# Kernel tuning notes

Measured on AMD Instinct MI355X. Metric: run time of the kernel, lower is better.

## Reference

```python
import jax, jax.numpy as jnp
import numpy as np

N_NODES = 10000
N_EDGES = 640000
NF = 64    # node_feature_size
EF = 64    # edge_feature_size
NH = 128   # node_hidden_size
EH = 128   # edge_hidden_size
CS = 128   # context_size


def _linear_init(key, fan_in, shape):
    bound = 1.0 / np.sqrt(fan_in)
    return jax.random.uniform(key, shape, jnp.float32, -bound, bound)


def setup_inputs() -> dict:
    key = jax.random.key(0)
    ks = jax.random.split(key, 20)
    node_feats = jax.random.normal(ks[0], (N_NODES, NF), jnp.float32)
    edge_feats = jax.random.normal(ks[1], (N_EDGES, EF), jnp.float32)
    src = jax.random.randint(ks[2], (N_EDGES,), 0, N_NODES, jnp.int32)
    dst = jax.random.randint(ks[3], (N_EDGES,), 0, N_NODES, jnp.int32)
    return {
        "node_feats": node_feats,
        "edge_feats": edge_feats,
        "W_node": _linear_init(ks[4], NF, (NF, NH)),
        "b_node": _linear_init(ks[5], NF, (NH,)),
        "W_edge": _linear_init(ks[6], NF + EF, (NF + EF, EH)),
        "b_edge": _linear_init(ks[7], NF + EF, (EH,)),
        "W_logit": _linear_init(ks[8], NH + EH, (NH + EH, 1)),
        "b_logit": _linear_init(ks[9], NH + EH, (1,)),
        "W_msg": _linear_init(ks[10], EH, (EH, CS)),
        "b_msg": _linear_init(ks[11], EH, (CS,)),
        "W_ih": _linear_init(ks[12], NH, (3 * NH, CS)),   # torch GRUCell weight_ih layout
        "W_hh": _linear_init(ks[13], NH, (3 * NH, NH)),
        "b_ih": _linear_init(ks[14], NH, (3 * NH,)),
        "b_hh": _linear_init(ks[15], NH, (3 * NH,)),
        "src": src,
        "dst": dst,
    }


def reference(node_feats, edge_feats, W_node, b_node, W_edge, b_edge,
              W_logit, b_logit, W_msg, b_msg, W_ih, W_hh, b_ih, b_hh,
              src, dst):
    n_nodes = node_feats.shape[0]
    # (1) embed nodes: h_v = LeakyReLU(Linear(f_v))
    h_v = jax.nn.leaky_relu(node_feats @ W_node + b_node)          # [N, NH]
    # (2) embed edges from [src node feats, edge feats]
    e_in = jnp.concatenate([node_feats[src], edge_feats], axis=1)  # [M, NF+EF]
    h_e = jax.nn.leaky_relu(e_in @ W_edge + b_edge)                # [M, EH]
    # raw messages T(h_w->v)
    m = h_e @ W_msg + b_msg                                        # [M, CS]
    # (3) attention logits from [src node hidden, edge hidden]
    l_in = jnp.concatenate([h_v[src], h_e], axis=1)                # [M, NH+EH]
    logit = jax.nn.leaky_relu(l_in @ W_logit + b_logit)            # [M, 1]
    # (4) edge softmax grouped by destination node
    lmax = jax.ops.segment_max(logit, dst, num_segments=n_nodes)   # [N, 1]
    ex = jnp.exp(logit - lmax[dst])
    den = jax.ops.segment_sum(ex, dst, num_segments=n_nodes)       # [N, 1]
    alpha = ex / den[dst]                                          # [M, 1]
    # (5) weighted segment-sum context, then elu
    C_v = jax.ops.segment_sum(alpha * m, dst, num_segments=n_nodes)  # [N, CS]
    C_v = jax.nn.elu(C_v)
    # (6) GRUCell(input=C_v, hidden=h_v), torch semantics, then ReLU
    gi = C_v @ W_ih.T + b_ih                                       # [N, 3*NH]
    gh = h_v @ W_hh.T + b_hh
    i_r, i_z, i_n = jnp.split(gi, 3, axis=1)
    h_r, h_z, h_n = jnp.split(gh, 3, axis=1)
    r = jax.nn.sigmoid(i_r + h_r)
    z = jax.nn.sigmoid(i_z + h_z)
    n = jnp.tanh(i_n + r * h_n)
    h_new = jax.nn.relu((1.0 - z) * n + z * h_v)                   # [N, NH]
    # update_edges=False -> return original edge feats alongside new node states
    return h_new, edge_feats
```

## Files before the change

kernel.cpp:

```cpp
#include <hip/hip_runtime.h>
#include <hip/hip_bf16.h>

typedef unsigned short u16;
typedef unsigned int u32;

typedef __attribute__((ext_vector_type(8))) short bf16x8;
typedef __attribute__((ext_vector_type(4))) float f32x4;

__device__ __forceinline__ u16 f2bf(float f) {
    u32 u = __float_as_uint(f);
    u32 r = ((u >> 16) & 1u) + 0x7fffu;
    return (u16)((u + r) >> 16);
}
__device__ __forceinline__ float bf2f(u16 u) {
    return __uint_as_float(((u32)u) << 16);
}
__device__ __forceinline__ float leaky(float x) { return x >= 0.f ? x : 0.01f * x; }

__global__ __launch_bounds__(256) void k_prep_transpose(
    const float* __restrict__ We, u16* __restrict__ WeT)
{
    int idx = blockIdx.x * 256 + threadIdx.x;
    int r = (idx >> 7) & 127;
    int c = idx & 127;
    WeT[c * 128 + r] = f2bf(We[r * 128 + c]);
}

__global__ __launch_bounds__(256) void k_csr_count(
    const int* __restrict__ dst, u32* __restrict__ deg, int nE)
{
    long e = (long)blockIdx.x * 256 + threadIdx.x;
    if (e >= nE) return;
    atomicAdd(&deg[dst[e]], 1u);
}

__global__ __launch_bounds__(256) void k_csr_scan(
    const u32* __restrict__ deg, u32* __restrict__ start,
    u32* __restrict__ cur, int nN)
{
    __shared__ u32 s[256];
    int t = threadIdx.x;
    int chunk = (nN + 255) / 256;
    int a = t * chunk;
    int b = a + chunk; if (b > nN) b = nN; if (a > nN) a = nN;
    u32 sum = 0;
    for (int i = a; i < b; i++) sum += deg[i];
    s[t] = sum;
    __syncthreads();
    for (int d = 1; d < 256; d <<= 1) {
        u32 v = (t >= d) ? s[t - d] : 0u;
        __syncthreads();
        s[t] += v;
        __syncthreads();
    }
    u32 base = (t == 0) ? 0u : s[t - 1];
    for (int i = a; i < b; i++) { start[i] = base; cur[i] = base; base += deg[i]; }
}

__global__ __launch_bounds__(256) void k_csr_scatter(
    const int* __restrict__ src, const int* __restrict__ dst,
    u32* __restrict__ cur, int* __restrict__ sEidG,
    int* __restrict__ sSrcG, int* __restrict__ sDstG, int nE)
{
    long e = (long)blockIdx.x * 256 + threadIdx.x;
    if (e >= nE) return;
    int d = dst[e];
    u32 p = atomicAdd(&cur[d], 1u);
    sEidG[p] = (int)e;
    sSrcG[p] = src[e];
    sDstG[p] = d;
}

__global__ __launch_bounds__(128) void k_node_embed(
    const float* __restrict__ nf, const float* __restrict__ Wn,
    const float* __restrict__ bn, const float* __restrict__ WL,
    float* __restrict__ h_v, float* __restrict__ g, int nN)
{
    __shared__ float sW[64][128];
    __shared__ float sF[8][64];
    __shared__ float sRed[2][8];
    int j = threadIdx.x;
    int n0 = blockIdx.x * 8;
    for (int i = 0; i < 64; i++) sW[i][j] = Wn[i * 128 + j];
    for (int t = j; t < 8 * 64; t += 128) {
        int n = t >> 6, k = t & 63;
        int nn = n0 + n; if (nn >= nN) nn = nN - 1;
        sF[n][k] = nf[(long)nn * 64 + k];
    }
    __syncthreads();
    float bj = bn[j];
    float wl = WL[j];
    int wv = j >> 6, ln = j & 63;
    float hval[8];
    for (int n = 0; n < 8; n++) {
        float acc = bj;
        #pragma unroll 16
        for (int k = 0; k < 64; k++) acc += sF[n][k] * sW[k][j];
        float h = leaky(acc);
        hval[n] = h;
        if (n0 + n < nN) h_v[(long)(n0 + n) * 128 + j] = h;
    }
    #pragma unroll
    for (int n = 0; n < 8; n++) {
        float part = hval[n] * wl;
        #pragma unroll
        for (int o = 1; o < 64; o <<= 1) part += __shfl_xor(part, o);
        if (ln == 0) sRed[wv][n] = part;
    }
    __syncthreads();
    if (j < 8 && n0 + j < nN) g[n0 + j] = sRed[0][j] + sRed[1][j];
}

template<bool WRITE_HE>
__global__ __launch_bounds__(256, 4) void k_edge_logit(
    const float* __restrict__ nf, const float* __restrict__ ef,
    const int* __restrict__ sEidG, const int* __restrict__ sSrcG,
    const u16* __restrict__ WeT, const float* __restrict__ be,
    const float* __restrict__ WL, const float* __restrict__ bL,
    const float* __restrict__ g,
    float* __restrict__ logitS, u16* __restrict__ heG,
    float* __restrict__ efOut, int nE)
{
    __shared__ u16 sW[64][136];
    __shared__ u16 sIn[64][136];
    __shared__ float sWL2[128];
    __shared__ float sG[64];
    __shared__ int sSrc[64];
    __shared__ int sEid[64];
    int tid = threadIdx.x;
    long p0 = (long)blockIdx.x * 64;
    if (tid < 64) {
        long p = p0 + tid; if (p >= nE) p = nE - 1;
        int eid = sEidG[p];
        int s = sSrcG[p];
        sEid[tid] = eid;
        sSrc[tid] = s;
        sG[tid] = g[s];
    } else if (tid < 192) {
        sWL2[tid - 64] = WL[64 + tid];
    }
    __syncthreads();
    for (int c = tid; c < 1024; c += 256) {
        int r = c >> 4, p = c & 15;
        *((uint4*)&sW[r][p * 8]) = *((const uint4*)(WeT + r * 128 + p * 8));
    }
    for (int c = tid; c < 2048; c += 256) {
        int e = c >> 5, p = c & 31;
        float4 v;
        if (p < 16) {
            v = *((const float4*)(nf + (long)sSrc[e] * 64 + p * 4));
        } else {
            v = *((const float4*)(ef + (long)sEid[e] * 64 + (p - 16) * 4));
            if (p0 + e < nE)
                *((float4*)(efOut + (long)sEid[e] * 64 + (p - 16) * 4)) = v;
        }
        u32 lo = (u32)f2bf(v.x) | ((u32)f2bf(v.y) << 16);
        u32 hi = (u32)f2bf(v.z) | ((u32)f2bf(v.w) << 16);
        *((u32*)&sIn[e][p * 4])     = lo;
        *((u32*)&sIn[e][p * 4 + 2]) = hi;
    }
    __syncthreads();

    int lane = tid & 63, w = tid >> 6;
    int nl = lane & 15, q = lane >> 4;
    int eA = w * 16 + nl;
    bf16x8 afr[4];
    #pragma unroll
    for (int s = 0; s < 4; s++)
        afr[s] = *((const bf16x8*)&sIn[eA][s * 32 + q * 8]);
    f32x4 acc[8];
    #pragma unroll
    for (int t = 0; t < 8; t++) acc[t] = (f32x4){0.f, 0.f, 0.f, 0.f};
    #pragma unroll
    for (int s = 0; s < 4; s++) {
        int k0 = s * 32 + q * 8;
        #pragma unroll
        for (int t = 0; t < 4; t++) {
            bf16x8 b = *((const bf16x8*)&sW[t * 16 + nl][k0]);
            acc[t] = __builtin_amdgcn_mfma_f32_16x16x32_bf16(afr[s], b, acc[t], 0, 0, 0);
        }
    }
    __syncthreads();
    for (int c = tid; c < 1024; c += 256) {
        int r = c >> 4, p = c & 15;
        *((uint4*)&sW[r][p * 8]) = *((const uint4*)(WeT + (64 + r) * 128 + p * 8));
    }
    __syncthreads();
    #pragma unroll
    for (int s = 0; s < 4; s++) {
        int k0 = s * 32 + q * 8;
        #pragma unroll
        for (int t = 0; t < 4; t++) {
            bf16x8 b = *((const bf16x8*)&sW[t * 16 + nl][k0]);
            acc[4 + t] = __builtin_amdgcn_mfma_f32_16x16x32_bf16(afr[s], b, acc[4 + t], 0, 0, 0);
        }
    }
    #pragma unroll
    for (int t = 0; t < 8; t++) {
        int col = t * 16 + nl;
        float bias = be[col];
        #pragma unroll
        for (int r = 0; r < 4; r++) {
            int e = w * 16 + q * 4 + r;
            sIn[e][col] = f2bf(leaky(acc[t][r] + bias));
        }
    }
    if (WRITE_HE) {
        #pragma unroll
        for (int i = 0; i < 4; i++) {
            int row = w * 16 + i * 4 + (lane >> 4);
            int ch = lane & 15;
            long pg = p0 + row;
            uint4 v4 = *((const uint4*)&sIn[row][ch * 8]);
            if (pg < nE) *((uint4*)(heG + pg * 128 + ch * 8)) = v4;
        }
    }
    int ew = lane >> 2, sub = lane & 3;
    int e = w * 16 + ew;
    float sum = 0.f;
    #pragma unroll
    for (int i = 0; i < 4; i++) {
        bf16x8 hv = *((const bf16x8*)&sIn[e][sub * 32 + i * 8]);
        #pragma unroll
        for (int jj = 0; jj < 8; jj++)
            sum += bf2f((u16)hv[jj]) * sWL2[sub * 32 + i * 8 + jj];
    }
    sum += __shfl_xor(sum, 1);
    sum += __shfl_xor(sum, 2);
    if (sub == 0 && p0 + e < nE) {
        float l = leaky(sum + sG[e] + bL[0]);
        logitS[p0 + e] = l;
    }
}

__global__ __launch_bounds__(256) void k_softmax_msg(
    const u32* __restrict__ start, const u32* __restrict__ deg,
    const u16* __restrict__ heG, float* __restrict__ logitS,
    float* __restrict__ A, int nN)
{
    __shared__ float sAl[4][1024];
    int wv = threadIdx.x >> 6, lane = threadIdx.x & 63;
    int v = blockIdx.x * 4 + wv;
    if (v >= nN) return;
    long base = (long)v * 128;
    u32 d = deg[v];
    if (d == 0) {
        A[base + lane] = 0.f;
        A[base + lane + 64] = 0.f;
        return;
    }
    u32 s0 = start[v];
    float mx = -3.402823e38f;
    for (u32 i = lane; i < d; i += 64) mx = fmaxf(mx, logitS[s0 + i]);
    #pragma unroll
    for (int o = 1; o < 64; o <<= 1) mx = fmaxf(mx, __shfl_xor(mx, o));
    float sum = 0.f;
    for (u32 i = lane; i < d; i += 64) {
        float e_ = __expf(logitS[s0 + i] - mx);
        sum += e_;
        if (i < 1024) sAl[wv][i] = e_;
        else logitS[s0 + i] = e_;
    }
    #pragma unroll
    for (int o = 1; o < 64; o <<= 1) sum += __shfl_xor(sum, o);
    float inv = 1.f / sum;
    float ax = 0.f, ay = 0.f;
    #pragma unroll 4
    for (u32 i = 0; i < d; i++) {
        float al = (i < 1024) ? sAl[wv][i] : logitS[s0 + i];
        u32 rw = *((const u32*)(heG + ((long)(s0 + i)) * 128 + lane * 2));
        ax += al * bf2f((u16)(rw & 0xffffu));
        ay += al * bf2f((u16)(rw >> 16));
    }
    A[base + lane * 2]     = ax * inv;
    A[base + lane * 2 + 1] = ay * inv;
}

__global__ __launch_bounds__(256) void k_softmax_node(
    const u32* __restrict__ start, const u32* __restrict__ deg,
    float* __restrict__ logitS, int nN)
{
    int v = blockIdx.x * 4 + (threadIdx.x >> 6);
    int lane = threadIdx.x & 63;
    if (v >= nN) return;
    u32 d = deg[v];
    if (d == 0) return;
    u32 s0 = start[v];
    float mx = -3.402823e38f;
    for (u32 i = lane; i < d; i += 64) mx = fmaxf(mx, logitS[s0 + i]);
    #pragma unroll
    for (int o = 1; o < 64; o <<= 1) mx = fmaxf(mx, __shfl_xor(mx, o));
    float sum = 0.f;
    for (u32 i = lane; i < d; i += 64) {
        float e = __expf(logitS[s0 + i] - mx);
        logitS[s0 + i] = e;
        sum += e;
    }
    #pragma unroll
    for (int o = 1; o < 64; o <<= 1) sum += __shfl_xor(sum, o);
    float inv = 1.f / sum;
    for (u32 i = lane; i < d; i += 64) logitS[s0 + i] *= inv;
}

__global__ __launch_bounds__(256) void k_msg_heavy(
    const float* __restrict__ nf, const float* __restrict__ ef,
    const int* __restrict__ sEidG, const int* __restrict__ sSrcG,
    const int* __restrict__ sDstG,
    const u16* __restrict__ WeT, const float* __restrict__ be,
    const float* __restrict__ alphaS,
    float* __restrict__ A, int nE)
{
    __shared__ u16 sW[128][136];
    __shared__ u16 sIn[64][136];
    __shared__ float sAlpha[64];
    __shared__ int sSrc[64];
    __shared__ int sEid[64];
    __shared__ int sDst[64];
    int tid = threadIdx.x;
    long p0 = (long)blockIdx.x * 64;
    if (tid < 64) {
        long p = p0 + tid;
        if (p < nE) {
            sEid[tid] = sEidG[p];
            sSrc[tid] = sSrcG[p];
            sDst[tid] = sDstG[p];
            sAlpha[tid] = alphaS[p];
        } else {
            sEid[tid] = sEidG[nE - 1];
            sSrc[tid] = sSrcG[nE - 1];
            sDst[tid] = sDstG[nE - 1];
            sAlpha[tid] = 0.f;
        }
    }
    __syncthreads();
    for (int c = tid; c < 2048; c += 256) {
        int r = c >> 4, pp = c & 15;
        *((uint4*)&sW[r][pp * 8]) = *((const uint4*)(WeT + r * 128 + pp * 8));
    }
    for (int c = tid; c < 64 * 32; c += 256) {
        int e = c >> 5, pp = c & 31;
        float4 v;
        if (pp < 16) v = *((const float4*)(nf + (long)sSrc[e] * 64 + pp * 4));
        else         v = *((const float4*)(ef + (long)sEid[e] * 64 + (pp - 16) * 4));
        u32 lo = (u32)f2bf(v.x) | ((u32)f2bf(v.y) << 16);
        u32 hi = (u32)f2bf(v.z) | ((u32)f2bf(v.w) << 16);
        *((u32*)&sIn[e][pp * 4])     = lo;
        *((u32*)&sIn[e][pp * 4 + 2]) = hi;
    }
    __syncthreads();

    int lane = tid & 63, w = tid >> 6;
    int nl = lane & 15, q = lane >> 4;
    f32x4 acc[8];
    #pragma unroll
    for (int t = 0; t < 8; t++) acc[t] = (f32x4){0.f, 0.f, 0.f, 0.f};
    int eA = w * 16 + nl;
    #pragma unroll
    for (int s = 0; s < 4; s++) {
        int k0 = s * 32 + q * 8;
        bf16x8 a = *((const bf16x8*)&sIn[eA][k0]);
        #pragma unroll
        for (int t = 0; t < 8; t++) {
            bf16x8 b = *((const bf16x8*)&sW[t * 16 + nl][k0]);
            acc[t] = __builtin_amdgcn_mfma_f32_16x16x32_bf16(a, b, acc[t], 0, 0, 0);
        }
    }
    #pragma unroll
    for (int t = 0; t < 8; t++) {
        int col = t * 16 + nl;
        float bias = be[col];
        #pragma unroll
        for (int r = 0; r < 4; r++) {
            int e = w * 16 + q * 4 + r;
            sIn[e][col] = f2bf(leaky(acc[t][r] + bias));
        }
    }
    int eb = w * 16;
    float sx = 0.f, sy = 0.f;
    int curd = sDst[eb];
    for (int i = 0; i < 16; i++) {
        int e = eb + i;
        float a = sAlpha[e];
        sx += a * bf2f(sIn[e][lane]);
        sy += a * bf2f(sIn[e][lane + 64]);
        int nxt = (i == 15) ? -1 : sDst[e + 1];
        if (nxt != curd) {
            atomicAdd(&A[(long)curd * 128 + lane], sx);
            atomicAdd(&A[(long)curd * 128 + lane + 64], sy);
            sx = 0.f; sy = 0.f;
            curd = nxt;
        }
    }
}

__global__ __launch_bounds__(128) void k_gru(
    const float* __restrict__ h_v, const float* __restrict__ A,
    const float* __restrict__ Wm, const float* __restrict__ bm,
    const u32* __restrict__ deg,
    const float* __restrict__ Wih, const float* __restrict__ Whh,
    const float* __restrict__ bih, const float* __restrict__ bhh,
    float* __restrict__ out, int nN)
{
    __shared__ float sA[8][128];
    __shared__ float sC[8][128];
    __shared__ float sH[8][128];
    int j = threadIdx.x;
    int n0 = blockIdx.x * 8;
    for (int n = 0; n < 8; n++) {
        int nn = n0 + n; if (nn >= nN) nn = nN - 1;
        sA[n][j] = A[(long)nn * 128 + j];
        sH[n][j] = h_v[(long)nn * 128 + j];
    }
    __syncthreads();
    float cc[8];
    {
        float bmj = bm[j];
        #pragma unroll
        for (int n = 0; n < 8; n++) cc[n] = bmj;
        for (int k = 0; k < 128; k++) {
            float wk = Wm[(long)k * 128 + j];
            #pragma unroll
            for (int n = 0; n < 8; n++) cc[n] += sA[n][k] * wk;
        }
    }
    for (int n = 0; n < 8; n++) {
        int nn = n0 + n; if (nn >= nN) nn = nN - 1;
        float c = cc[n];
        sC[n][j] = (deg[nn] > 0u) ? (c > 0.f ? c : __expf(c) - 1.f) : 0.f;
    }
    __syncthreads();
    float gi[3][8], gh[3][8];
    #pragma unroll
    for (int g = 0; g < 3; g++) {
        float bi = bih[g * 128 + j];
        float bh = bhh[g * 128 + j];
        #pragma unroll
        for (int n = 0; n < 8; n++) { gi[g][n] = bi; gh[g][n] = bh; }
    }
    for (int k = 0; k < 128; k += 4) {
        float4 cv[8], hv[8];
        #pragma unroll
        for (int n = 0; n < 8; n++) {
            cv[n] = *(const float4*)&sC[n][k];
            hv[n] = *(const float4*)&sH[n][k];
        }
        #pragma unroll
        for (int g = 0; g < 3; g++) {
            float4 wi = *((const float4*)(Wih + (long)(g * 128 + j) * 128 + k));
            float4 wh = *((const float4*)(Whh + (long)(g * 128 + j) * 128 + k));
            #pragma unroll
            for (int n = 0; n < 8; n++) {
                gi[g][n] += wi.x * cv[n].x + wi.y * cv[n].y + wi.z * cv[n].z + wi.w * cv[n].w;
                gh[g][n] += wh.x * hv[n].x + wh.y * hv[n].y + wh.z * hv[n].z + wh.w * hv[n].w;
            }
        }
    }
    #pragma unroll
    for (int n = 0; n < 8; n++) {
        if (n0 + n >= nN) break;
        float r = 1.f / (1.f + __expf(-(gi[0][n] + gh[0][n])));
        float z = 1.f / (1.f + __expf(-(gi[1][n] + gh[1][n])));
        float nn = tanhf(gi[2][n] + r * gh[2][n]);
        float h = (1.f - z) * nn + z * sH[n][j];
        out[(long)(n0 + n) * 128 + j] = (h > 0.f ? h : 0.f);
    }
}

extern "C" void kernel_launch(void* const* d_in, const int* in_sizes, int n_in,
                              void* d_out, int out_size, void* d_ws, size_t ws_size,
                              hipStream_t stream) {
    const float* nf  = (const float*)d_in[0];
    const float* ef  = (const float*)d_in[1];
    const float* Wn  = (const float*)d_in[2];
    const float* bn  = (const float*)d_in[3];
    const float* We  = (const float*)d_in[4];
    const float* be  = (const float*)d_in[5];
    const float* WL  = (const float*)d_in[6];
    const float* bL  = (const float*)d_in[7];
    const float* Wm  = (const float*)d_in[8];
    const float* bm  = (const float*)d_in[9];
    const float* Wih = (const float*)d_in[10];
    const float* Whh = (const float*)d_in[11];
    const float* bih = (const float*)d_in[12];
    const float* bhh = (const float*)d_in[13];
    const int* src = (const int*)d_in[14];
    const int* dst = (const int*)d_in[15];
    float* out = (float*)d_out;

    int nN = in_sizes[0] / 64;
    int nE = in_sizes[1] / 64;

    size_t o = 0;
    auto nxt = [&](size_t b) { size_t p = o; o += (b + 255) & ~(size_t)255; return p; };
    size_t o_hv    = nxt((size_t)nN * 128 * 4);
    size_t o_g     = nxt((size_t)nN * 4);
    size_t o_logit = nxt((size_t)nE * 4);
    size_t o_A     = nxt((size_t)nN * 128 * 4);
    size_t o_deg   = nxt((size_t)nN * 4);
    size_t o_start = nxt((size_t)nN * 4);
    size_t o_cur   = nxt((size_t)nN * 4);
    size_t o_eid   = nxt((size_t)nE * 4);
    size_t o_srcS  = nxt((size_t)nE * 4);
    size_t o_dstS  = nxt((size_t)nE * 4);
    size_t o_WeT   = nxt((size_t)128 * 128 * 2);
    size_t o_he    = nxt((size_t)nE * 128 * 2);
    bool lite = (o <= ws_size);

    char* w = (char*)d_ws;
    float* h_v    = (float*)(w + o_hv);
    float* g      = (float*)(w + o_g);
    float* logitS = (float*)(w + o_logit);
    float* A      = (float*)(w + o_A);
    u32*   deg    = (u32*)(w + o_deg);
    u32*   start  = (u32*)(w + o_start);
    u32*   cur    = (u32*)(w + o_cur);
    int*   sEid   = (int*)(w + o_eid);
    int*   sSrcS  = (int*)(w + o_srcS);
    int*   sDstS  = (int*)(w + o_dstS);
    u16*   WeT    = (u16*)(w + o_WeT);
    u16*   heG    = (u16*)(w + o_he);
    float* efOut  = out + (size_t)nN * 128;

    if (lite) {
        hipMemsetAsync(deg, 0, (size_t)nN * 4, stream);
    } else {
        hipMemsetAsync(A, 0, o_start - o_A, stream);
    }

    int gN8   = (nN + 7) / 8;
    int gN4   = (nN + 3) / 4;
    int gE64  = (nE + 63) / 64;
    int gE256 = (nE + 255) / 256;

    k_prep_transpose<<<64, 256, 0, stream>>>(We, WeT);
    k_csr_count<<<gE256, 256, 0, stream>>>(dst, deg, nE);
    k_csr_scan<<<1, 256, 0, stream>>>(deg, start, cur, nN);
    k_csr_scatter<<<gE256, 256, 0, stream>>>(src, dst, cur, sEid, sSrcS, sDstS, nE);
    k_node_embed<<<gN8, 128, 0, stream>>>(nf, Wn, bn, WL, h_v, g, nN);
    if (lite) {
        k_edge_logit<true><<<gE64, 256, 0, stream>>>(
            nf, ef, sEid, sSrcS, WeT, be, WL, bL, g, logitS, heG, efOut, nE);
        k_softmax_msg<<<gN4, 256, 0, stream>>>(start, deg, heG, logitS, A, nN);
    } else {
        k_edge_logit<false><<<gE64, 256, 0, stream>>>(
            nf, ef, sEid, sSrcS, WeT, be, WL, bL, g, logitS, heG, efOut, nE);
        k_softmax_node<<<gN4, 256, 0, stream>>>(start, deg, logitS, nN);
        k_msg_heavy<<<gE64, 256, 0, stream>>>(nf, ef, sEid, sSrcS, sDstS,
                                              WeT, be, logitS, A, nE);
    }
    k_gru<<<gN8, 128, 0, stream>>>(h_v, A, Wm, bm, deg,
                                   Wih, Whh, bih, bhh, out, nN);
}
```

Before: 746.8 us.

## Recompute edge hidden in message kernel instead of materializing it globally

Removes the bf16 edge-hidden buffer and the per-node softmax-message kernel, always using logit, node-softmax and a recomputing message kernel. The logit dot product is fused into registers with lane shuffles instead of going through shared memory. Sorted src/dst copies are dropped in favour of indirect lookups through the sorted edge id, and the message kernel now loads weights in two halves to cut shared memory. This trades a large global write and read for a second edge GEMM and atomic accumulation.

```diff
diff --git a/kernel.cpp b/kernel.cpp
--- a/kernel.cpp
+++ b/kernel.cpp
@@ -58,17 +58,14 @@
 }
 
 __global__ __launch_bounds__(256) void k_csr_scatter(
-    const int* __restrict__ src, const int* __restrict__ dst,
-    u32* __restrict__ cur, int* __restrict__ sEidG,
-    int* __restrict__ sSrcG, int* __restrict__ sDstG, int nE)
+    const int* __restrict__ dst, u32* __restrict__ cur,
+    int* __restrict__ sEidG, int nE)
 {
     long e = (long)blockIdx.x * 256 + threadIdx.x;
     if (e >= nE) return;
     int d = dst[e];
     u32 p = atomicAdd(&cur[d], 1u);
     sEidG[p] = (int)e;
-    sSrcG[p] = src[e];
-    sDstG[p] = d;
 }
 
 __global__ __launch_bounds__(128) void k_node_embed(
@@ -111,15 +108,13 @@
     if (j < 8 && n0 + j < nN) g[n0 + j] = sRed[0][j] + sRed[1][j];
 }
 
-template<bool WRITE_HE>
 __global__ __launch_bounds__(256, 4) void k_edge_logit(
     const float* __restrict__ nf, const float* __restrict__ ef,
-    const int* __restrict__ sEidG, const int* __restrict__ sSrcG,
+    const int* __restrict__ sEidG, const int* __restrict__ src,
     const u16* __restrict__ WeT, const float* __restrict__ be,
     const float* __restrict__ WL, const float* __restrict__ bL,
     const float* __restrict__ g,
-    float* __restrict__ logitS, u16* __restrict__ heG,
-    float* __restrict__ efOut, int nE)
+    float* __restrict__ logitS, float* __restrict__ efOut, int nE)
 {
     __shared__ u16 sW[64][136];
     __shared__ u16 sIn[64][136];
@@ -132,7 +127,7 @@
     if (tid < 64) {
         long p = p0 + tid; if (p >= nE) p = nE - 1;
         int eid = sEidG[p];
-        int s = sSrcG[p];
+        int s = src[eid];
         sEid[tid] = eid;
         sSrc[tid] = s;
         sG[tid] = g[s];
@@ -195,85 +190,30 @@
             acc[4 + t] = __builtin_amdgcn_mfma_f32_16x16x32_bf16(afr[s], b, acc[4 + t], 0, 0, 0);
         }
     }
+    float ls0 = 0.f, ls1 = 0.f, ls2 = 0.f, ls3 = 0.f;
     #pragma unroll
     for (int t = 0; t < 8; t++) {
         int col = t * 16 + nl;
         float bias = be[col];
-        #pragma unroll
-        for (int r = 0; r < 4; r++) {
-            int e = w * 16 + q * 4 + r;
-            sIn[e][col] = f2bf(leaky(acc[t][r] + bias));
-        }
-    }
-    if (WRITE_HE) {
-        #pragma unroll
-        for (int i = 0; i < 4; i++) {
-            int row = w * 16 + i * 4 + (lane >> 4);
-            int ch = lane & 15;
-            long pg = p0 + row;
-            uint4 v4 = *((const uint4*)&sIn[row][ch * 8]);
-            if (pg < nE) *((uint4*)(heG + pg * 128 + ch * 8)) = v4;
-        }
-    }
-    int ew = lane >> 2, sub = lane & 3;
-    int e = w * 16 + ew;
-    float sum = 0.f;
-    #pragma unroll
-    for (int i = 0; i < 4; i++) {
-        bf16x8 hv = *((const bf16x8*)&sIn[e][sub * 32 + i * 8]);
-        #pragma unroll
-        for (int jj = 0; jj < 8; jj++)
-            sum += bf2f((u16)hv[jj]) * sWL2[sub * 32 + i * 8 + jj];
-    }
-    sum += __shfl_xor(sum, 1);
-    sum += __shfl_xor(sum, 2);
-    if (sub == 0 && p0 + e < nE) {
-        float l = leaky(sum + sG[e] + bL[0]);
-        logitS[p0 + e] = l;
-    }
-}
-
-__global__ __launch_bounds__(256) void k_softmax_msg(
-    const u32* __restrict__ start, const u32* __restrict__ deg,
-    const u16* __restrict__ heG, float* __restrict__ logitS,
-    float* __restrict__ A, int nN)
-{
-    __shared__ float sAl[4][1024];
-    int wv = threadIdx.x >> 6, lane = threadIdx.x & 63;
-    int v = blockIdx.x * 4 + wv;
-    if (v >= nN) return;
-    long base = (long)v * 128;
-    u32 d = deg[v];
-    if (d == 0) {
-        A[base + lane] = 0.f;
-        A[base + lane + 64] = 0.f;
-        return;
-    }
-    u32 s0 = start[v];
-    float mx = -3.402823e38f;
-    for (u32 i = lane; i < d; i += 64) mx = fmaxf(mx, logitS[s0 + i]);
-    #pragma unroll
-    for (int o = 1; o < 64; o <<= 1) mx = fmaxf(mx, __shfl_xor(mx, o));
-    float sum = 0.f;
-    for (u32 i = lane; i < d; i += 64) {
-        float e_ = __expf(logitS[s0 + i] - mx);
-        sum += e_;
-        if (i < 1024) sAl[wv][i] = e_;
-        else logitS[s0 + i] = e_;
-    }
-    #pragma unroll
-    for (int o = 1; o < 64; o <<= 1) sum += __shfl_xor(sum, o);
-    float inv = 1.f / sum;
-    float ax = 0.f, ay = 0.f;
-    #pragma unroll 4
-    for (u32 i = 0; i < d; i++) {
-        float al = (i < 1024) ? sAl[wv][i] : logitS[s0 + i];
-        u32 rw = *((const u32*)(heG + ((long)(s0 + i)) * 128 + lane * 2));
-        ax += al * bf2f((u16)(rw & 0xffffu));
-        ay += al * bf2f((u16)(rw >> 16));
-    }
-    A[base + lane * 2]     = ax * inv;
-    A[base + lane * 2 + 1] = ay * inv;
+        float wl2 = sWL2[col];
+        ls0 += leaky(acc[t][0] + bias) * wl2;
+        ls1 += leaky(acc[t][1] + bias) * wl2;
+        ls2 += leaky(acc[t][2] + bias) * wl2;
+        ls3 += leaky(acc[t][3] + bias) * wl2;
+    }
+    #pragma unroll
+    for (int o = 1; o < 16; o <<= 1) {
+        ls0 += __shfl_xor(ls0, o);
+        ls1 += __shfl_xor(ls1, o);
+        ls2 += __shfl_xor(ls2, o);
+        ls3 += __shfl_xor(ls3, o);
+    }
+    if (nl < 4) {
+        float lv = nl == 0 ? ls0 : nl == 1 ? ls1 : nl == 2 ? ls2 : ls3;
+        int e = w * 16 + q * 4 + nl;
+        long pg = p0 + e;
+        if (pg < nE) logitS[pg] = leaky(lv + sG[e] + bL[0]);
+    }
 }
 
 __global__ __launch_bounds__(256) void k_softmax_node(
@@ -302,15 +242,15 @@
     for (u32 i = lane; i < d; i += 64) logitS[s0 + i] *= inv;
 }
 
-__global__ __launch_bounds__(256) void k_msg_heavy(
+__global__ __launch_bounds__(256, 4) void k_msg(
     const float* __restrict__ nf, const float* __restrict__ ef,
-    const int* __restrict__ sEidG, const int* __restrict__ sSrcG,
-    const int* __restrict__ sDstG,
+    const int* __restrict__ sEidG, const int* __restrict__ src,
+    const int* __restrict__ dst,
     const u16* __restrict__ WeT, const float* __restrict__ be,
     const float* __restrict__ alphaS,
     float* __restrict__ A, int nE)
 {
-    __shared__ u16 sW[128][136];
+    __shared__ u16 sW[64][136];
     __shared__ u16 sIn[64][136];
     __shared__ float sAlpha[64];
     __shared__ int sSrc[64];
@@ -320,24 +260,20 @@
     long p0 = (long)blockIdx.x * 64;
     if (tid < 64) {
         long p = p0 + tid;
-        if (p < nE) {
-            sEid[tid] = sEidG[p];
-            sSrc[tid] = sSrcG[p];
-            sDst[tid] = sDstG[p];
-            sAlpha[tid] = alphaS[p];
-        } else {
-            sEid[tid] = sEidG[nE - 1];
-            sSrc[tid] = sSrcG[nE - 1];
-            sDst[tid] = sDstG[nE - 1];
-            sAlpha[tid] = 0.f;
-        }
-    }
-    __syncthreads();
-    for (int c = tid; c < 2048; c += 256) {
+        bool ok = p < nE;
+        if (!ok) p = nE - 1;
+        int eid = sEidG[p];
+        sEid[tid] = eid;
+        sSrc[tid] = src[eid];
+        sDst[tid] = dst[eid];
+        sAlpha[tid] = ok ? alphaS[p] : 0.f;
+    }
+    __syncthreads();
+    for (int c = tid; c < 1024; c += 256) {
         int r = c >> 4, pp = c & 15;
         *((uint4*)&sW[r][pp * 8]) = *((const uint4*)(WeT + r * 128 + pp * 8));
     }
-    for (int c = tid; c < 64 * 32; c += 256) {
+    for (int c = tid; c < 2048; c += 256) {
         int e = c >> 5, pp = c & 31;
         float4 v;
         if (pp < 16) v = *((const float4*)(nf + (long)sSrc[e] * 64 + pp * 4));
@@ -351,18 +287,36 @@
 
     int lane = tid & 63, w = tid >> 6;
     int nl = lane & 15, q = lane >> 4;
+    int eA = w * 16 + nl;
+    bf16x8 afr[4];
+    #pragma unroll
+    for (int s = 0; s < 4; s++)
+        afr[s] = *((const bf16x8*)&sIn[eA][s * 32 + q * 8]);
     f32x4 acc[8];
     #pragma unroll
     for (int t = 0; t < 8; t++) acc[t] = (f32x4){0.f, 0.f, 0.f, 0.f};
-    int eA = w * 16 + nl;
     #pragma unroll
     for (int s = 0; s < 4; s++) {
         int k0 = s * 32 + q * 8;
-        bf16x8 a = *((const bf16x8*)&sIn[eA][k0]);
-        #pragma unroll
-        for (int t = 0; t < 8; t++) {
+        #pragma unroll
+        for (int t = 0; t < 4; t++) {
             bf16x8 b = *((const bf16x8*)&sW[t * 16 + nl][k0]);
-            acc[t] = __builtin_amdgcn_mfma_f32_16x16x32_bf16(a, b, acc[t], 0, 0, 0);
+            acc[t] = __builtin_amdgcn_mfma_f32_16x16x32_bf16(afr[s], b, acc[t], 0, 0, 0);
+        }
+    }
+    __syncthreads();
+    for (int c = tid; c < 1024; c += 256) {
+        int r = c >> 4, pp = c & 15;
+        *((uint4*)&sW[r][pp * 8]) = *((const uint4*)(WeT + (64 + r) * 128 + pp * 8));
+    }
+    __syncthreads();
+    #pragma unroll
+    for (int s = 0; s < 4; s++) {
+        int k0 = s * 32 + q * 8;
+        #pragma unroll
+        for (int t = 0; t < 4; t++) {
+            bf16x8 b = *((const bf16x8*)&sW[t * 16 + nl][k0]);
+            acc[4 + t] = __builtin_amdgcn_mfma_f32_16x16x32_bf16(afr[s], b, acc[4 + t], 0, 0, 0);
         }
     }
     #pragma unroll
@@ -500,11 +454,8 @@
     size_t o_start = nxt((size_t)nN * 4);
     size_t o_cur   = nxt((size_t)nN * 4);
     size_t o_eid   = nxt((size_t)nE * 4);
-    size_t o_srcS  = nxt((size_t)nE * 4);
-    size_t o_dstS  = nxt((size_t)nE * 4);
     size_t o_WeT   = nxt((size_t)128 * 128 * 2);
-    size_t o_he    = nxt((size_t)nE * 128 * 2);
-    bool lite = (o <= ws_size);
+    (void)o;
 
     char* w = (char*)d_ws;
     float* h_v    = (float*)(w + o_hv);
@@ -515,17 +466,10 @@
     u32*   start  = (u32*)(w + o_start);
     u32*   cur    = (u32*)(w + o_cur);
     int*   sEid   = (int*)(w + o_eid);
-    int*   sSrcS  = (int*)(w + o_srcS);
-    int*   sDstS  = (int*)(w + o_dstS);
     u16*   WeT    = (u16*)(w + o_WeT);
-    u16*   heG    = (u16*)(w + o_he);
     float* efOut  = out + (size_t)nN * 128;
 
-    if (lite) {
-        hipMemsetAsync(deg, 0, (size_t)nN * 4, stream);
-    } else {
-        hipMemsetAsync(A, 0, o_start - o_A, stream);
-    }
+    hipMemsetAsync(A, 0, o_start - o_A, stream);
 
     int gN8   = (nN + 7) / 8;
     int gN4   = (nN + 3) / 4;
@@ -535,19 +479,13 @@
     k_prep_transpose<<<64, 256, 0, stream>>>(We, WeT);
     k_csr_count<<<gE256, 256, 0, stream>>>(dst, deg, nE);
     k_csr_scan<<<1, 256, 0, stream>>>(deg, start, cur, nN);
-    k_csr_scatter<<<gE256, 256, 0, stream>>>(src, dst, cur, sEid, sSrcS, sDstS, nE);
+    k_csr_scatter<<<gE256, 256, 0, stream>>>(dst, cur, sEid, nE);
     k_node_embed<<<gN8, 128, 0, stream>>>(nf, Wn, bn, WL, h_v, g, nN);
-    if (lite) {
-        k_edge_logit<true><<<gE64, 256, 0, stream>>>(
-            nf, ef, sEid, sSrcS, WeT, be, WL, bL, g, logitS, heG, efOut, nE);
-        k_softmax_msg<<<gN4, 256, 0, stream>>>(start, deg, heG, logitS, A, nN);
-    } else {
-        k_edge_logit<false><<<gE64, 256, 0, stream>>>(
-            nf, ef, sEid, sSrcS, WeT, be, WL, bL, g, logitS, heG, efOut, nE);
-        k_softmax_node<<<gN4, 256, 0, stream>>>(start, deg, logitS, nN);
-        k_msg_heavy<<<gE64, 256, 0, stream>>>(nf, ef, sEid, sSrcS, sDstS,
-                                              WeT, be, logitS, A, nE);
-    }
+    k_edge_logit<<<gE64, 256, 0, stream>>>(
+        nf, ef, sEid, src, WeT, be, WL, bL, g, logitS, efOut, nE);
+    k_softmax_node<<<gN4, 256, 0, stream>>>(start, deg, logitS, nN);
+    k_msg<<<gE64, 256, 0, stream>>>(nf, ef, sEid, src, dst, WeT, be,
+                                    logitS, A, nE);
     k_gru<<<gN8, 128, 0, stream>>>(h_v, A, Wm, bm, deg,
                                    Wih, Whh, bih, bhh, out, nN);
 }
```

After: 821.5 us. 1.1x slower.
